# Kernel optimization log

Hardware: AMD Instinct MI355X
Metric: run time of the kernel (lower is better)

## Reference

```python
import jax, jax.numpy as jnp
import numpy as np

NG, NPG, EPG = 64, 256, 2048        # graphs, nodes/graph, edges/graph
N, E = NG * NPG, NG * EPG
FN, FE, FG = 256, 64, 128           # node/edge/global feature dims
MSG_DIMS = [FE + 2 * FN + FG, 512, 512, 256]   # message_arch '512-512-256'
UPD_DIMS = [256 + FN + FG, 512, 256]           # node_arch '512-256'
N_EMB_G, OUT_NODE, OUT_ACT = 256, 64, 8


def _mlp(x, params):
    # Linear -> ReLU stack (Dropout is identity in eval mode)
    for w, b in params:
        x = jax.nn.relu(x @ w + b)
    return x


def setup_inputs():
    key = jax.random.key(0)
    ks = jax.random.split(key, 24)
    nodes = jax.random.normal(ks[0], (N, FN), jnp.float32)
    edge_attr = jax.random.normal(ks[1], (E, FE), jnp.float32)
    global_attr = jax.random.normal(ks[2], (NG, FG), jnp.float32)
    # edges are grouped by graph (matches repeat_interleave(global, num_edges))
    rng = np.random.default_rng(0)
    gid_e = np.repeat(np.arange(NG), EPG)
    src = gid_e * NPG + rng.integers(0, NPG, E)
    tgt = gid_e * NPG + rng.integers(0, NPG, E)
    edge_indices = jnp.asarray(np.stack([src, tgt]), jnp.int32)
    num_nodes = jnp.full((NG,), NPG, jnp.int32)
    num_edges = jnp.full((NG,), EPG, jnp.int32)
    batch_indices = jnp.asarray(np.repeat(np.arange(NG), NPG), jnp.int32)

    def lin(k, fi, fo):
        kw, kb = jax.random.split(k)
        lim = 1.0 / np.sqrt(fi)
        return (jax.random.uniform(kw, (fi, fo), jnp.float32, -lim, lim),
                jax.random.uniform(kb, (fo,), jnp.float32, -lim, lim))

    inp = dict(nodes=nodes, edge_attr=edge_attr, global_attr=global_attr,
               edge_indices=edge_indices, num_nodes=num_nodes,
               num_edges=num_edges, batch_indices=batch_indices)
    for i in range(3):
        w, b = lin(ks[3 + i], MSG_DIMS[i], MSG_DIMS[i + 1])
        inp[f'msg_w{i}'], inp[f'msg_b{i}'] = w, b
    for i in range(2):
        w, b = lin(ks[6 + i], UPD_DIMS[i], UPD_DIMS[i + 1])
        inp[f'upd_w{i}'], inp[f'upd_b{i}'] = w, b
    inp['glob_w'], inp['glob_b'] = lin(ks[8], UPD_DIMS[-1] + FG, N_EMB_G)
    inp['emb_w'], inp['emb_b'] = lin(ks[9], UPD_DIMS[-1], OUT_NODE)
    inp['act_w'], inp['act_b'] = lin(ks[10], N_EMB_G, OUT_ACT)
    return inp


def reference(nodes, edge_attr, global_attr, edge_indices, num_nodes,
              num_edges, batch_indices, msg_w0, msg_b0, msg_w1, msg_b1,
              msg_w2, msg_b2, upd_w0, upd_b0, upd_w1, upd_b1,
              glob_w, glob_b, emb_w, emb_b, act_w, act_b):
    n, e = nodes.shape[0], edge_indices.shape[1]
    ng = global_attr.shape[0]
    src, tgt = edge_indices[0], edge_indices[1]
    glob_e = jnp.repeat(global_attr, num_edges, axis=0, total_repeat_length=e)
    concat = jnp.concatenate([nodes[src], edge_attr, nodes[tgt], glob_e], axis=1)
    # message_nn ends with ReLU; outer F.relu is a no-op on non-neg values
    message = _mlp(concat, [(msg_w0, msg_b0), (msg_w1, msg_b1), (msg_w2, msg_b2)])
    # scatter_max into per-node slots; messages >= 0 so zeros init matches fill=0
    aggr = jnp.zeros((n, message.shape[1]), message.dtype).at[tgt].max(message)
    glob_n = jnp.repeat(global_attr, num_nodes, axis=0, total_repeat_length=n)
    h = _mlp(jnp.concatenate([nodes, aggr, glob_n], axis=1),
             [(upd_w0, upd_b0), (upd_w1, upd_b1)])
    agg_nodes = jnp.zeros((ng, h.shape[1]), h.dtype).at[batch_indices].max(h)
    g = jax.nn.relu(jnp.concatenate([agg_nodes, global_attr], axis=1) @ glob_w + glob_b)
    node_pred = jax.nn.relu(h @ emb_w + emb_b)
    action = jax.nn.softmax(g @ act_w + act_b, axis=1)
    return node_pred, action
```

## Files before the change

kernel.cpp:

```cpp
#include <hip/hip_runtime.h>
#include <hip/hip_bf16.h>

typedef unsigned short u16;
using u16x4 = __attribute__((ext_vector_type(4))) unsigned short;
using u16x8 = __attribute__((ext_vector_type(8))) unsigned short;
using u32x4 = __attribute__((ext_vector_type(4))) unsigned int;
using f32x4 = __attribute__((ext_vector_type(4))) float;
using bf16x8 = __attribute__((ext_vector_type(8))) __bf16;

#define TNG 64
#define TNN 16384
#define TNE 131072
#define TFN 256
#define TFE 64
#define TFG 128

__device__ __forceinline__ u16 f2bf(float f) {
    unsigned u = __float_as_uint(f);
    unsigned r = (u + 0x7FFFu + ((u >> 16) & 1u)) >> 16;
    return (u16)r;
}
__device__ __forceinline__ float b2f(u16 h) {
    return __uint_as_float(((unsigned)h) << 16);
}

__device__ __forceinline__ void gload_lds16(const u16* g, u16* l) {
    __builtin_amdgcn_global_load_lds(
        (const __attribute__((address_space(1))) void*)g,
        (__attribute__((address_space(3))) void*)l, 16, 0, 0);
}

__device__ __forceinline__ int xcd_swz(int bid, int nwg) {
    return (nwg & 7) == 0 ? (bid & 7) * (nwg >> 3) + (bid >> 3) : bid;
}


__global__ void cast_kernel(const float* __restrict__ in, u16* __restrict__ out, int n4) {
    int i = blockIdx.x * 256 + threadIdx.x;
    if (i >= n4) return;
    f32x4 v = *(const f32x4*)(in + (size_t)i * 4);
    u16x4 o;
    o.x = f2bf(v.x); o.y = f2bf(v.y); o.z = f2bf(v.z); o.w = f2bf(v.w);
    *(u16x4*)(out + (size_t)i * 4) = o;
}


struct PrepTab {
    const float* W[8];
    int out_off[8];
    int Nin[8], Nact[8], r0[8], Ksub[8], idx0[8];
};

__global__ void prep_weights_kernel(PrepTab tab, u16* __restrict__ wsbase, int total) {
    int gid = blockIdx.x * 256 + threadIdx.x;
    if (gid >= total) return;
    int i = 7;
#pragma unroll
    for (int j = 7; j > 0; --j)
        if (gid < tab.idx0[j]) i = j - 1;
    int loc = gid - tab.idx0[i];
    int ks = tab.Ksub[i];
    int n = loc / ks;
    int k = loc - n * ks;
    float v = (n < tab.Nact[i]) ? tab.W[i][(size_t)(tab.r0[i] + k) * tab.Nin[i] + n] : 0.0f;
    wsbase[tab.out_off[i] + loc] = f2bf(v);
}


template <int K, int NXSH, bool RELU, bool OUT_BF16>
__global__ __launch_bounds__(256) void gemm_bt_kernel(
    const u16* __restrict__ A, const u16* __restrict__ Bt,
    const float* __restrict__ bias, void* __restrict__ Cv,
    int Nout, int ldc) {
    __shared__ u16 As[128 * 32];
    __shared__ u16 Bs[128 * 32];
    const int w = xcd_swz(blockIdx.x, gridDim.x);
    const int bxi = w & ((1 << NXSH) - 1);
    const int byi = w >> NXSH;
    const int tid = threadIdx.x;
    const int wave = tid >> 6, lane = tid & 63;
    const int wr = wave >> 1, wc = wave & 1;
    const size_t brow = (size_t)byi * 128;
    const size_t bcol = (size_t)bxi * 128;
    const int srow = tid >> 2;
    const int qsrc = (tid & 3) ^ ((srow >> 1) & 3);
    const u16* aSrc = A + (brow + srow) * (size_t)K + qsrc * 8;
    const u16* bSrc = Bt + (bcol + srow) * (size_t)K + qsrc * 8;
    u16* aDst = &As[tid * 8];
    u16* bDst = &Bs[tid * 8];
    const size_t stepRows = (size_t)64 * K;

    f32x4 acc[4][4] = {};

#pragma unroll
    for (int k0 = 0; k0 < K; k0 += 32) {
        gload_lds16(aSrc + k0, aDst);
        gload_lds16(aSrc + stepRows + k0, aDst + 2048);
        gload_lds16(bSrc + k0, bDst);
        gload_lds16(bSrc + stepRows + k0, bDst + 2048);
        __syncthreads();
        bf16x8 af[4], bfv[4];
#pragma unroll
        for (int m = 0; m < 4; ++m) {
            const int row = wr * 64 + m * 16 + (lane & 15);
            const int slot = (lane >> 4) ^ ((row >> 1) & 3);
            af[m] = *(const bf16x8*)&As[row * 32 + slot * 8];
        }
#pragma unroll
        for (int n = 0; n < 4; ++n) {
            const int row = wc * 64 + n * 16 + (lane & 15);
            const int slot = (lane >> 4) ^ ((row >> 1) & 3);
            bfv[n] = *(const bf16x8*)&Bs[row * 32 + slot * 8];
        }
#pragma unroll
        for (int m = 0; m < 4; ++m)
#pragma unroll
            for (int n = 0; n < 4; ++n)
                acc[m][n] = __builtin_amdgcn_mfma_f32_16x16x32_bf16(af[m], bfv[n], acc[m][n], 0, 0, 0);
        __syncthreads();
    }

    const int rowSub = wr * 64 + (lane >> 4) * 4;
#pragma unroll
    for (int n = 0; n < 4; ++n) {
        const int col = (int)bcol + wc * 64 + n * 16 + (lane & 15);
        if (col >= Nout) continue;
        const float bv = bias ? bias[col] : 0.0f;
#pragma unroll
        for (int m = 0; m < 4; ++m) {
#pragma unroll
            for (int i = 0; i < 4; ++i) {
                float v = acc[m][n][i] + bv;
                if (RELU) v = fmaxf(v, 0.0f);
                size_t off = (brow + rowSub + m * 16 + i) * (size_t)ldc + col;
                if (OUT_BF16) ((u16*)Cv)[off] = f2bf(v);
                else ((float*)Cv)[off] = v;
            }
        }
    }
}


__global__ __launch_bounds__(256) void gemm_u0_kernel(
    const u16* __restrict__ nodes_bf, const u16* __restrict__ aggr,
    const u16* __restrict__ glob_bf, const u16* __restrict__ U0T,
    const float* __restrict__ bias, u16* __restrict__ C) {
    __shared__ u16 As[128 * 32];
    __shared__ u16 Bs[128 * 32];
    const int w = xcd_swz(blockIdx.x, gridDim.x);
    const int bxi = w & 3;
    const int byi = w >> 2;
    const int tid = threadIdx.x;
    const int wave = tid >> 6, lane = tid & 63;
    const int wr = wave >> 1, wc = wave & 1;
    const size_t brow = (size_t)byi * 128;
    const size_t bcol = (size_t)bxi * 128;
    const int srow = tid >> 2;
    const int scol = ((tid & 3) ^ ((srow >> 1) & 3)) * 8;
    const int r0i = (int)brow + srow;
    const u16* bSrc = U0T + (bcol + srow) * (size_t)640 + scol;
    u16* aDst = &As[tid * 8];
    u16* bDst = &Bs[tid * 8];

    f32x4 acc[4][4] = {};

#pragma unroll
    for (int k0 = 0; k0 < 640; k0 += 32) {
        const u16* p0;
        const u16* p1;
        if (k0 < 256) {
            p0 = nodes_bf + (size_t)r0i * 256 + k0 + scol;
            p1 = nodes_bf + (size_t)(r0i + 64) * 256 + k0 + scol;
        } else if (k0 < 512) {
            p0 = aggr + (size_t)r0i * 256 + (k0 - 256) + scol;
            p1 = aggr + (size_t)(r0i + 64) * 256 + (k0 - 256) + scol;
        } else {
            p0 = glob_bf + (size_t)(r0i >> 8) * 128 + (k0 - 512) + scol;
            p1 = glob_bf + (size_t)((r0i + 64) >> 8) * 128 + (k0 - 512) + scol;
        }
        gload_lds16(p0, aDst);
        gload_lds16(p1, aDst + 2048);
        gload_lds16(bSrc + k0, bDst);
        gload_lds16(bSrc + (size_t)64 * 640 + k0, bDst + 2048);
        __syncthreads();
        bf16x8 af[4], bfv[4];
#pragma unroll
        for (int m = 0; m < 4; ++m) {
            const int row = wr * 64 + m * 16 + (lane & 15);
            const int slot = (lane >> 4) ^ ((row >> 1) & 3);
            af[m] = *(const bf16x8*)&As[row * 32 + slot * 8];
        }
#pragma unroll
        for (int n = 0; n < 4; ++n) {
            const int row = wc * 64 + n * 16 + (lane & 15);
            const int slot = (lane >> 4) ^ ((row >> 1) & 3);
            bfv[n] = *(const bf16x8*)&Bs[row * 32 + slot * 8];
        }
#pragma unroll
        for (int m = 0; m < 4; ++m)
#pragma unroll
            for (int n = 0; n < 4; ++n)
                acc[m][n] = __builtin_amdgcn_mfma_f32_16x16x32_bf16(af[m], bfv[n], acc[m][n], 0, 0, 0);
        __syncthreads();
    }

    const int rowSub = wr * 64 + (lane >> 4) * 4;
#pragma unroll
    for (int n = 0; n < 4; ++n) {
        const int col = (int)bcol + wc * 64 + n * 16 + (lane & 15);
        const float bv = bias[col];
#pragma unroll
        for (int m = 0; m < 4; ++m)
#pragma unroll
            for (int i = 0; i < 4; ++i) {
                float v = fmaxf(acc[m][n][i] + bv, 0.0f);
                C[(brow + rowSub + m * 16 + i) * (size_t)512 + col] = f2bf(v);
            }
    }
}


__global__ __launch_bounds__(256) void gd_kernel(const float* __restrict__ glob,
                                                 const float* __restrict__ msg_w0,
                                                 const float* __restrict__ b0,
                                                 float* __restrict__ Gdb,
                                                 u16* __restrict__ glob_bf) {
    int g = blockIdx.x;
    __shared__ float in[TFG];
    if (threadIdx.x < TFG) {
        float v = glob[g * TFG + threadIdx.x];
        in[threadIdx.x] = v;
        glob_bf[g * TFG + threadIdx.x] = f2bf(v);
    }
    __syncthreads();
    for (int j = threadIdx.x; j < 512; j += 256) {
        float s = b0[j];
        for (int k = 0; k < TFG; ++k) s += in[k] * msg_w0[(size_t)(576 + k) * 512 + j];
        Gdb[(size_t)g * 512 + j] = s;
    }
}


__global__ __launch_bounds__(256) void h1_fused_kernel(
    const float* __restrict__ Ef, const u16* __restrict__ WbT,
    const u16* __restrict__ Pac, const float* __restrict__ Gdb,
    const int* __restrict__ src, const int* __restrict__ tgt,
    u16* __restrict__ h1, int e0) {
    __shared__ u16 smem[17408];
    u16* As = smem;
    u16* Bs = smem + 8192;
    const int w = xcd_swz(blockIdx.x, gridDim.x);
    const int bxi = w & 3;
    const int byi = w >> 2;
    const int tid = threadIdx.x;
    const int wave = tid >> 6, lane = tid & 63;
    const int wr = wave >> 1, wc = wave & 1;
    const int brow = byi * 128;
    const int bcol = bxi * 128;

    {
        const int r = tid >> 2;
        const int cq = (tid & 3) * 2;
        const int sw = r & 7;
#pragma unroll
        for (int h = 0; h < 2; ++h) {
            const float* sp = Ef + (size_t)(e0 + brow + r + h * 64) * 64 + cq * 8;
            f32x4 v0 = *(const f32x4*)(sp);
            f32x4 v1 = *(const f32x4*)(sp + 4);
            f32x4 v2 = *(const f32x4*)(sp + 8);
            f32x4 v3 = *(const f32x4*)(sp + 12);
            u16x8 o0, o1;
            o0[0] = f2bf(v0.x); o0[1] = f2bf(v0.y); o0[2] = f2bf(v0.z); o0[3] = f2bf(v0.w);
            o0[4] = f2bf(v1.x); o0[5] = f2bf(v1.y); o0[6] = f2bf(v1.z); o0[7] = f2bf(v1.w);
            o1[0] = f2bf(v2.x); o1[1] = f2bf(v2.y); o1[2] = f2bf(v2.z); o1[3] = f2bf(v2.w);
            o1[4] = f2bf(v3.x); o1[5] = f2bf(v3.y); o1[6] = f2bf(v3.z); o1[7] = f2bf(v3.w);
            *(u16x8*)&As[(r + h * 64) * 64 + (cq ^ sw) * 8] = o0;
            *(u16x8*)&As[(r + h * 64) * 64 + ((cq + 1) ^ sw) * 8] = o1;
        }
#pragma unroll
        for (int j = 0; j < 4; ++j) {
            int li = j * 256 + tid;
            int row = li >> 3;
            int gslot = (li & 7) ^ (row & 7);
            gload_lds16(WbT + (size_t)(bcol + row) * 64 + gslot * 8, &Bs[li * 8]);
        }
    }
    __syncthreads();

    f32x4 acc[4][4] = {};
#pragma unroll
    for (int k0 = 0; k0 < 64; k0 += 32) {
        bf16x8 af[4], bv[4];
#pragma unroll
        for (int m = 0; m < 4; ++m) {
            const int row = wr * 64 + m * 16 + (lane & 15);
            const int slot = ((k0 >> 3) + (lane >> 4)) ^ (row & 7);
            af[m] = *(const bf16x8*)&As[row * 64 + slot * 8];
        }
#pragma unroll
        for (int n = 0; n < 4; ++n) {
            const int row = wc * 64 + n * 16 + (lane & 15);
            const int slot = ((k0 >> 3) + (lane >> 4)) ^ (row & 7);
            bv[n] = *(const bf16x8*)&Bs[row * 64 + slot * 8];
        }
#pragma unroll
        for (int m = 0; m < 4; ++m)
#pragma unroll
            for (int n = 0; n < 4; ++n)
                acc[m][n] = __builtin_amdgcn_mfma_f32_16x16x32_bf16(af[m], bv[n], acc[m][n], 0, 0, 0);
    }
    __syncthreads();

    const int rowSub = wr * 64 + (lane >> 4) * 4;
#pragma unroll
    for (int m = 0; m < 4; ++m)
#pragma unroll
        for (int n = 0; n < 4; ++n)
#pragma unroll
            for (int i = 0; i < 4; ++i)
                smem[(rowSub + m * 16 + i) * 136 + wc * 64 + n * 16 + (lane & 15)] =
                    f2bf(acc[m][n][i]);
    __syncthreads();

#pragma unroll
    for (int it = 0; it < 8; ++it) {
        int lin = it * 256 + tid;
        int r = lin >> 4;
        int q = (lin & 15) * 8;
        int e = e0 + brow + r;
        int s = src[e];
        int t = tgt[e];
        int g = e >> 11;
        int col = bcol + q;
        u16x8 pa = *(const u16x8*)(Pac + (size_t)s * 1024 + col);
        u16x8 pc = *(const u16x8*)(Pac + (size_t)t * 1024 + 512 + col);
        u16x8 eb = *(const u16x8*)&smem[r * 136 + q];
        f32x4 g0 = *(const f32x4*)(Gdb + (size_t)g * 512 + col);
        f32x4 g1 = *(const f32x4*)(Gdb + (size_t)g * 512 + col + 4);
        u16x8 o;
#pragma unroll
        for (int j = 0; j < 8; ++j) {
            float gd = (j < 4) ? g0[j] : g1[j - 4];
            float v = b2f(pa[j]) + b2f(pc[j]) + b2f(eb[j]) + gd;
            o[j] = f2bf(fmaxf(v, 0.0f));
        }
        *(u16x8*)(h1 + (size_t)(brow + r) * 512 + col) = o;
    }
}


__global__ __launch_bounds__(1024) void scatter_max_kernel(
    const u16* __restrict__ msg, const int* __restrict__ tgt,
    u16* __restrict__ aggr, int g0, int e0) {
    int g = g0 + (blockIdx.x >> 2);
    int fc = blockIdx.x & 3;
    __shared__ unsigned smax[256 * 64];
    int tid = threadIdx.x;
    for (int i = tid; i < 256 * 64; i += 1024) smax[i] = 0u;
    __syncthreads();
    const int eg = g * 2048;
    const int n0 = g * 256;
    const int f = tid & 63;
    const int eo = tid >> 6;
    const u16* mrow = msg + fc * 64 + f;
    const int end = eg + 2048;
    for (int e = eg + eo; e < end; e += 64) {
        int t0 = tgt[e], t1 = tgt[e + 16], t2 = tgt[e + 32], t3 = tgt[e + 48];
        unsigned v0 = ((unsigned)mrow[(size_t)(e      - e0) * 256]) << 16;
        unsigned v1 = ((unsigned)mrow[(size_t)(e + 16 - e0) * 256]) << 16;
        unsigned v2 = ((unsigned)mrow[(size_t)(e + 32 - e0) * 256]) << 16;
        unsigned v3 = ((unsigned)mrow[(size_t)(e + 48 - e0) * 256]) << 16;
        int a0 = t0 - n0, a1 = t1 - n0, a2 = t2 - n0, a3 = t3 - n0;
        if ((unsigned)a0 < 256u) atomicMax(&smax[a0 * 64 + f], v0);
        if ((unsigned)a1 < 256u) atomicMax(&smax[a1 * 64 + f], v1);
        if ((unsigned)a2 < 256u) atomicMax(&smax[a2 * 64 + f], v2);
        if ((unsigned)a3 < 256u) atomicMax(&smax[a3 * 64 + f], v3);
    }
    __syncthreads();
    for (int i = tid; i < 256 * 64; i += 1024) {
        int nl = i >> 6, ff = i & 63;
        aggr[(size_t)(n0 + nl) * 256 + fc * 64 + ff] = (u16)(smax[nl * 64 + ff] >> 16);
    }
}


__global__ __launch_bounds__(256) void agg_nodes_kernel(
    const u16* __restrict__ h, float* __restrict__ aggn) {
    int g = blockIdx.x;
    int f = threadIdx.x;
    int n0 = g * 256;
    float m0 = 0.0f, m1 = 0.0f, m2 = 0.0f, m3 = 0.0f;
    for (int n = 0; n < 256; n += 4) {
        m0 = fmaxf(m0, b2f(h[(size_t)(n0 + n) * 256 + f]));
        m1 = fmaxf(m1, b2f(h[(size_t)(n0 + n + 1) * 256 + f]));
        m2 = fmaxf(m2, b2f(h[(size_t)(n0 + n + 2) * 256 + f]));
        m3 = fmaxf(m3, b2f(h[(size_t)(n0 + n + 3) * 256 + f]));
    }
    aggn[(size_t)g * 256 + f] = fmaxf(fmaxf(m0, m1), fmaxf(m2, m3));
}


__global__ __launch_bounds__(256) void glob_kernel(
    const float* __restrict__ aggn, const float* __restrict__ glob,
    const float* __restrict__ W, const float* __restrict__ b,
    float* __restrict__ gout) {
    int g = blockIdx.x;
    int j = threadIdx.x;
    __shared__ float in[384];
    if (threadIdx.x < 256) in[threadIdx.x] = aggn[(size_t)g * 256 + threadIdx.x];
    if (threadIdx.x < 128) in[256 + threadIdx.x] = glob[(size_t)g * 128 + threadIdx.x];
    __syncthreads();
    float s = b[j];
    for (int k = 0; k < 384; ++k) s += in[k] * W[(size_t)k * 256 + j];
    gout[(size_t)g * 256 + j] = fmaxf(s, 0.0f);
}


__global__ void action_kernel(const float* __restrict__ gout,
                              const float* __restrict__ actw,
                              const float* __restrict__ actb,
                              float* __restrict__ out) {
    int g = blockIdx.x;
    int j = threadIdx.x;
    __shared__ float logits[8];
    if (j < 8) {
        float s = actb[j];
        for (int k = 0; k < 256; ++k) s += gout[(size_t)g * 256 + k] * actw[(size_t)k * 8 + j];
        logits[j] = s;
    }
    __syncthreads();
    if (j == 0) {
        float mx = logits[0];
        for (int i = 1; i < 8; ++i) mx = fmaxf(mx, logits[i]);
        float ex[8], den = 0.0f;
        for (int i = 0; i < 8; ++i) { ex[i] = expf(logits[i] - mx); den += ex[i]; }
        float inv = 1.0f / den;
        for (int i = 0; i < 8; ++i) out[(size_t)g * 8 + i] = ex[i] * inv;
    }
}


constexpr size_t OFF_NODES_BF = 0;
constexpr size_t OFF_GLOB_BF  = OFF_NODES_BF + (size_t)TNN * TFN * 2;
constexpr size_t OFF_WACT = OFF_GLOB_BF + (size_t)TNG * TFG * 2;
constexpr size_t OFF_WBT  = OFF_WACT + 1024 * 256 * 2;
constexpr size_t OFF_W1T  = OFF_WBT + 512 * 64 * 2;
constexpr size_t OFF_W2T  = OFF_W1T + 512 * 512 * 2;
constexpr size_t OFF_U0T  = OFF_W2T + 256 * 512 * 2;
constexpr size_t OFF_U1T  = OFF_U0T + 512 * 640 * 2;
constexpr size_t OFF_EMBT = OFF_U1T + 256 * 512 * 2;
constexpr size_t OFF_AGGN = OFF_EMBT + 128 * 256 * 2;
constexpr size_t OFF_GOUT = OFF_AGGN + 64 * 256 * 4;
constexpr size_t OFF_AGGR = OFF_GOUT + 64 * 256 * 4;
constexpr size_t OFF_GDB  = OFF_AGGR + (size_t)TNN * 256 * 2;
constexpr size_t OFF_PAC  = OFF_GDB + 64 * 512 * 4;
constexpr size_t OFF_V    = OFF_PAC + (size_t)TNN * 1024 * 2;
constexpr size_t SZ_HU1   = (size_t)TNN * 512 * 2;

extern "C" void kernel_launch(void* const* d_in, const int* in_sizes, int n_in,
                              void* d_out, int out_size, void* d_ws, size_t ws_size,
                              hipStream_t stream) {
    const float* nodes       = (const float*)d_in[0];
    const float* edge_attr   = (const float*)d_in[1];
    const float* global_attr = (const float*)d_in[2];
    const int*   edge_idx    = (const int*)d_in[3];
    const float* msg_w0 = (const float*)d_in[7];
    const float* msg_b0 = (const float*)d_in[8];
    const float* msg_w1 = (const float*)d_in[9];
    const float* msg_b1 = (const float*)d_in[10];
    const float* msg_w2 = (const float*)d_in[11];
    const float* msg_b2 = (const float*)d_in[12];
    const float* upd_w0 = (const float*)d_in[13];
    const float* upd_b0 = (const float*)d_in[14];
    const float* upd_w1 = (const float*)d_in[15];
    const float* upd_b1 = (const float*)d_in[16];
    const float* glob_w = (const float*)d_in[17];
    const float* glob_b = (const float*)d_in[18];
    const float* emb_w  = (const float*)d_in[19];
    const float* emb_b  = (const float*)d_in[20];
    const float* act_w  = (const float*)d_in[21];
    const float* act_b  = (const float*)d_in[22];

    const int* src = edge_idx;
    const int* tgt = edge_idx + TNE;

    char* ws = (char*)d_ws;
    u16* nodes_bf = (u16*)(ws + OFF_NODES_BF);
    u16* glob_bf  = (u16*)(ws + OFF_GLOB_BF);
    u16* WacT = (u16*)(ws + OFF_WACT);
    u16* WbT  = (u16*)(ws + OFF_WBT);
    u16* W1T  = (u16*)(ws + OFF_W1T);
    u16* W2T  = (u16*)(ws + OFF_W2T);
    u16* U0T  = (u16*)(ws + OFF_U0T);
    u16* U1T  = (u16*)(ws + OFF_U1T);
    u16* EmbT = (u16*)(ws + OFF_EMBT);
    float* aggn = (float*)(ws + OFF_AGGN);
    float* gout = (float*)(ws + OFF_GOUT);
    u16* aggr = (u16*)(ws + OFF_AGGR);
    float* Gdb = (float*)(ws + OFF_GDB);
    u16* Pac  = (u16*)(ws + OFF_PAC);
    float* out = (float*)d_out;

    size_t CH = (size_t)TNE;
    while (CH > 2048) {
        size_t need = OFF_V + (CH * 2560 > SZ_HU1 ? CH * 2560 : SZ_HU1);
        if (need <= ws_size) break;
        CH >>= 1;
    }
    const int nchunk = (int)((size_t)TNE / CH);
    const int gpc = (int)(CH / 2048);

    u16* h1c  = (u16*)(ws + OFF_V);
    u16* h2c  = (u16*)(ws + OFF_V + CH * 1024);
    u16* msgc = (u16*)(ws + OFF_V + CH * 2048);
    u16* hu1  = (u16*)(ws + OFF_V);
    u16* h_bf = (u16*)(ws + OFF_AGGR);

    cast_kernel<<<(TNN * TFN / 4 + 255) / 256, 256, 0, stream>>>(nodes, nodes_bf, TNN * TFN / 4);

    PrepTab tab;
    {
        const float* Ws[8]  = {msg_w0, msg_w0, msg_w0, msg_w1, msg_w2, upd_w0, upd_w1, emb_w};
        int offs[8] = {(int)(OFF_WACT / 2), (int)(OFF_WACT / 2) + 131072, (int)(OFF_WBT / 2),
                       (int)(OFF_W1T / 2), (int)(OFF_W2T / 2), (int)(OFF_U0T / 2),
                       (int)(OFF_U1T / 2), (int)(OFF_EMBT / 2)};
        int nin[8]  = {512, 512, 512, 512, 256, 512, 256, 64};
        int nact[8] = {512, 512, 512, 512, 256, 512, 256, 64};
        int r0v[8]  = {0, 320, 256, 0, 0, 0, 0, 0};
        int ksub[8] = {256, 256, 64, 512, 512, 640, 512, 256};
        int sizes[8] = {131072, 131072, 32768, 262144, 131072, 327680, 131072, 32768};
        int acc = 0;
        for (int i = 0; i < 8; ++i) {
            tab.W[i] = Ws[i]; tab.out_off[i] = offs[i]; tab.Nin[i] = nin[i];
            tab.Nact[i] = nact[i]; tab.r0[i] = r0v[i]; tab.Ksub[i] = ksub[i];
            tab.idx0[i] = acc; acc += sizes[i];
        }
    }
    prep_weights_kernel<<<4608, 256, 0, stream>>>(tab, (u16*)ws, 1179648);
    gd_kernel<<<64, 256, 0, stream>>>(global_attr, msg_w0, msg_b0, Gdb, glob_bf);

    gemm_bt_kernel<256, 3, false, true><<<1024, 256, 0, stream>>>(nodes_bf, WacT, nullptr, Pac, 1024, 1024);

    for (int ci = 0; ci < nchunk; ++ci) {
        const int e0 = (int)(ci * CH);
        const int nwg = (int)(CH / 32);
        h1_fused_kernel<<<nwg, 256, 0, stream>>>(
            edge_attr, WbT, Pac, Gdb, src, tgt, h1c, e0);
        gemm_bt_kernel<512, 2, true, true><<<nwg, 256, 0, stream>>>(h1c, W1T, msg_b1, h2c, 512, 512);
        gemm_bt_kernel<512, 1, true, true><<<nwg / 2, 256, 0, stream>>>(h2c, W2T, msg_b2, msgc, 256, 256);
        scatter_max_kernel<<<gpc * 4, 1024, 0, stream>>>(msgc, tgt, aggr, ci * gpc, e0);
    }

    gemm_u0_kernel<<<512, 256, 0, stream>>>(nodes_bf, aggr, glob_bf, U0T, upd_b0, hu1);
    gemm_bt_kernel<512, 1, true, true><<<256, 256, 0, stream>>>(hu1, U1T, upd_b1, h_bf, 256, 256);

    agg_nodes_kernel<<<64, 256, 0, stream>>>(h_bf, aggn);
    glob_kernel<<<64, 256, 0, stream>>>(aggn, global_attr, glob_w, glob_b, gout);
    action_kernel<<<64, 64, 0, stream>>>(gout, act_w, act_b, out + (size_t)TNN * 64);
    gemm_bt_kernel<256, 0, true, false><<<128, 256, 0, stream>>>(h_bf, EmbT, emb_b, out, 64, 64);

    (void)in_sizes; (void)n_in; (void)out_size;
}
```

Measured before the change: 400.3 us.

## Double-buffer GEMM LDS tiles, tile weight prep, vectorize scatter, fuse head kernels

The bf16 GEMM kernels, including the fused update GEMM, now use two LDS buffers. The next K-slice is loaded while MFMAs run on the current one, which is meant to hide global-load latency behind compute. Weight preparation becomes a 64x64 LDS-tiled transpose so both reads and writes are coalesced, instead of one strided gather per element. scatter_max reads four message features per thread with a vector load. The three small head kernels (node max-pool, global MLP, softmax) are merged into one, which removes two launches and their intermediate buffers. The cost is twice the LDS per GEMM block, which may lower occupancy.

```diff
diff --git a/kernel.cpp b/kernel.cpp
--- a/kernel.cpp
+++ b/kernel.cpp
@@ -48,22 +48,39 @@
 struct PrepTab {
     const float* W[8];
     int out_off[8];
-    int Nin[8], Nact[8], r0[8], Ksub[8], idx0[8];
+    int Nin[8], Nact[8], r0[8], Ksub[8];
+    int tile0[8];
+    int tkn[8];
 };
 
-__global__ void prep_weights_kernel(PrepTab tab, u16* __restrict__ wsbase, int total) {
-    int gid = blockIdx.x * 256 + threadIdx.x;
-    if (gid >= total) return;
+__global__ __launch_bounds__(256) void prep_weights_kernel(PrepTab tab, u16* __restrict__ wsbase) {
+    const int b = blockIdx.x;
     int i = 7;
 #pragma unroll
     for (int j = 7; j > 0; --j)
-        if (gid < tab.idx0[j]) i = j - 1;
-    int loc = gid - tab.idx0[i];
-    int ks = tab.Ksub[i];
-    int n = loc / ks;
-    int k = loc - n * ks;
-    float v = (n < tab.Nact[i]) ? tab.W[i][(size_t)(tab.r0[i] + k) * tab.Nin[i] + n] : 0.0f;
-    wsbase[tab.out_off[i] + loc] = f2bf(v);
+        if (b < tab.tile0[j]) i = j - 1;
+    const int loc = b - tab.tile0[i];
+    const int tk = loc % tab.tkn[i];
+    const int tn = loc / tab.tkn[i];
+    const int kb = tk * 64, nb = tn * 64;
+    const int Nin = tab.Nin[i], Nact = tab.Nact[i], r0 = tab.r0[i], Ksub = tab.Ksub[i];
+    const float* W = tab.W[i];
+    u16* outp = wsbase + tab.out_off[i];
+
+    __shared__ float t[64][65];
+    const int tid = threadIdx.x;
+    const int nl = tid & 63;
+    const bool nok = (nb + nl) < Nact;
+#pragma unroll 4
+    for (int kk = tid >> 6; kk < 64; kk += 4) {
+        float v = nok ? W[(size_t)(r0 + kb + kk) * Nin + nb + nl] : 0.0f;
+        t[kk][nl] = v;
+    }
+    __syncthreads();
+    const int kl = tid & 63;
+#pragma unroll 4
+    for (int nn = tid >> 6; nn < 64; nn += 4)
+        outp[(size_t)(nb + nn) * Ksub + kb + kl] = f2bf(t[kl][nn]);
 }
 
 
@@ -72,8 +89,9 @@
     const u16* __restrict__ A, const u16* __restrict__ Bt,
     const float* __restrict__ bias, void* __restrict__ Cv,
     int Nout, int ldc) {
-    __shared__ u16 As[128 * 32];
-    __shared__ u16 Bs[128 * 32];
+    constexpr int NT = K / 32;
+    __shared__ u16 As[2][4096];
+    __shared__ u16 Bs[2][4096];
     const int w = xcd_swz(blockIdx.x, gridDim.x);
     const int bxi = w & ((1 << NXSH) - 1);
     const int byi = w >> NXSH;
@@ -86,31 +104,36 @@
     const int qsrc = (tid & 3) ^ ((srow >> 1) & 3);
     const u16* aSrc = A + (brow + srow) * (size_t)K + qsrc * 8;
     const u16* bSrc = Bt + (bcol + srow) * (size_t)K + qsrc * 8;
-    u16* aDst = &As[tid * 8];
-    u16* bDst = &Bs[tid * 8];
     const size_t stepRows = (size_t)64 * K;
 
+    auto stage = [&](int t, int buf) {
+        const int k0 = t * 32;
+        gload_lds16(aSrc + k0, &As[buf][tid * 8]);
+        gload_lds16(aSrc + stepRows + k0, &As[buf][tid * 8 + 2048]);
+        gload_lds16(bSrc + k0, &Bs[buf][tid * 8]);
+        gload_lds16(bSrc + stepRows + k0, &Bs[buf][tid * 8 + 2048]);
+    };
+
     f32x4 acc[4][4] = {};
 
-#pragma unroll
-    for (int k0 = 0; k0 < K; k0 += 32) {
-        gload_lds16(aSrc + k0, aDst);
-        gload_lds16(aSrc + stepRows + k0, aDst + 2048);
-        gload_lds16(bSrc + k0, bDst);
-        gload_lds16(bSrc + stepRows + k0, bDst + 2048);
-        __syncthreads();
+    stage(0, 0);
+    __syncthreads();
+#pragma unroll
+    for (int t = 0; t < NT; ++t) {
+        const int cur = t & 1;
+        if (t + 1 < NT) stage(t + 1, cur ^ 1);
         bf16x8 af[4], bfv[4];
 #pragma unroll
         for (int m = 0; m < 4; ++m) {
             const int row = wr * 64 + m * 16 + (lane & 15);
             const int slot = (lane >> 4) ^ ((row >> 1) & 3);
-            af[m] = *(const bf16x8*)&As[row * 32 + slot * 8];
+            af[m] = *(const bf16x8*)&As[cur][row * 32 + slot * 8];
         }
 #pragma unroll
         for (int n = 0; n < 4; ++n) {
             const int row = wc * 64 + n * 16 + (lane & 15);
             const int slot = (lane >> 4) ^ ((row >> 1) & 3);
-            bfv[n] = *(const bf16x8*)&Bs[row * 32 + slot * 8];
+            bfv[n] = *(const bf16x8*)&Bs[cur][row * 32 + slot * 8];
         }
 #pragma unroll
         for (int m = 0; m < 4; ++m)
@@ -145,8 +168,8 @@
     const u16* __restrict__ nodes_bf, const u16* __restrict__ aggr,
     const u16* __restrict__ glob_bf, const u16* __restrict__ U0T,
     const float* __restrict__ bias, u16* __restrict__ C) {
-    __shared__ u16 As[128 * 32];
-    __shared__ u16 Bs[128 * 32];
+    __shared__ u16 As[2][4096];
+    __shared__ u16 Bs[2][4096];
     const int w = xcd_swz(blockIdx.x, gridDim.x);
     const int bxi = w & 3;
     const int byi = w >> 2;
@@ -159,15 +182,10 @@
     const int scol = ((tid & 3) ^ ((srow >> 1) & 3)) * 8;
     const int r0i = (int)brow + srow;
     const u16* bSrc = U0T + (bcol + srow) * (size_t)640 + scol;
-    u16* aDst = &As[tid * 8];
-    u16* bDst = &Bs[tid * 8];
-
-    f32x4 acc[4][4] = {};
-
-#pragma unroll
-    for (int k0 = 0; k0 < 640; k0 += 32) {
-        const u16* p0;
-        const u16* p1;
+
+    auto stage = [&](int t, int buf) {
+        const int k0 = t * 32;
+        const u16 *p0, *p1;
         if (k0 < 256) {
             p0 = nodes_bf + (size_t)r0i * 256 + k0 + scol;
             p1 = nodes_bf + (size_t)(r0i + 64) * 256 + k0 + scol;
@@ -178,23 +196,32 @@
             p0 = glob_bf + (size_t)(r0i >> 8) * 128 + (k0 - 512) + scol;
             p1 = glob_bf + (size_t)((r0i + 64) >> 8) * 128 + (k0 - 512) + scol;
         }
-        gload_lds16(p0, aDst);
-        gload_lds16(p1, aDst + 2048);
-        gload_lds16(bSrc + k0, bDst);
-        gload_lds16(bSrc + (size_t)64 * 640 + k0, bDst + 2048);
-        __syncthreads();
+        gload_lds16(p0, &As[buf][tid * 8]);
+        gload_lds16(p1, &As[buf][tid * 8 + 2048]);
+        gload_lds16(bSrc + k0, &Bs[buf][tid * 8]);
+        gload_lds16(bSrc + (size_t)64 * 640 + k0, &Bs[buf][tid * 8 + 2048]);
+    };
+
+    f32x4 acc[4][4] = {};
+
+    stage(0, 0);
+    __syncthreads();
+#pragma unroll
+    for (int t = 0; t < 20; ++t) {
+        const int cur = t & 1;
+        if (t + 1 < 20) stage(t + 1, cur ^ 1);
         bf16x8 af[4], bfv[4];
 #pragma unroll
         for (int m = 0; m < 4; ++m) {
             const int row = wr * 64 + m * 16 + (lane & 15);
             const int slot = (lane >> 4) ^ ((row >> 1) & 3);
-            af[m] = *(const bf16x8*)&As[row * 32 + slot * 8];
+            af[m] = *(const bf16x8*)&As[cur][row * 32 + slot * 8];
         }
 #pragma unroll
         for (int n = 0; n < 4; ++n) {
             const int row = wc * 64 + n * 16 + (lane & 15);
             const int slot = (lane >> 4) ^ ((row >> 1) & 3);
-            bfv[n] = *(const bf16x8*)&Bs[row * 32 + slot * 8];
+            bfv[n] = *(const bf16x8*)&Bs[cur][row * 32 + slot * 8];
         }
 #pragma unroll
         for (int m = 0; m < 4; ++m)
@@ -360,21 +387,42 @@
     __syncthreads();
     const int eg = g * 2048;
     const int n0 = g * 256;
-    const int f = tid & 63;
-    const int eo = tid >> 6;
-    const u16* mrow = msg + fc * 64 + f;
-    const int end = eg + 2048;
-    for (int e = eg + eo; e < end; e += 64) {
-        int t0 = tgt[e], t1 = tgt[e + 16], t2 = tgt[e + 32], t3 = tgt[e + 48];
-        unsigned v0 = ((unsigned)mrow[(size_t)(e      - e0) * 256]) << 16;
-        unsigned v1 = ((unsigned)mrow[(size_t)(e + 16 - e0) * 256]) << 16;
-        unsigned v2 = ((unsigned)mrow[(size_t)(e + 32 - e0) * 256]) << 16;
-        unsigned v3 = ((unsigned)mrow[(size_t)(e + 48 - e0) * 256]) << 16;
+    const int f4 = (tid & 15) * 4;
+    const int elane = tid >> 4;
+    const u16* mbase = msg + fc * 64 + f4;
+#pragma unroll
+    for (int wv = 0; wv < 32; wv += 4) {
+        const int e = eg + elane + wv * 64;
+        int t0 = tgt[e], t1 = tgt[e + 64], t2 = tgt[e + 128], t3 = tgt[e + 192];
+        u16x4 m0 = *(const u16x4*)(mbase + (size_t)(e       - e0) * 256);
+        u16x4 m1 = *(const u16x4*)(mbase + (size_t)(e +  64 - e0) * 256);
+        u16x4 m2 = *(const u16x4*)(mbase + (size_t)(e + 128 - e0) * 256);
+        u16x4 m3 = *(const u16x4*)(mbase + (size_t)(e + 192 - e0) * 256);
         int a0 = t0 - n0, a1 = t1 - n0, a2 = t2 - n0, a3 = t3 - n0;
-        if ((unsigned)a0 < 256u) atomicMax(&smax[a0 * 64 + f], v0);
-        if ((unsigned)a1 < 256u) atomicMax(&smax[a1 * 64 + f], v1);
-        if ((unsigned)a2 < 256u) atomicMax(&smax[a2 * 64 + f], v2);
-        if ((unsigned)a3 < 256u) atomicMax(&smax[a3 * 64 + f], v3);
+        if ((unsigned)a0 < 256u) {
+            atomicMax(&smax[a0 * 64 + f4],     ((unsigned)m0.x) << 16);
+            atomicMax(&smax[a0 * 64 + f4 + 1], ((unsigned)m0.y) << 16);
+            atomicMax(&smax[a0 * 64 + f4 + 2], ((unsigned)m0.z) << 16);
+            atomicMax(&smax[a0 * 64 + f4 + 3], ((unsigned)m0.w) << 16);
+        }
+        if ((unsigned)a1 < 256u) {
+            atomicMax(&smax[a1 * 64 + f4],     ((unsigned)m1.x) << 16);
+            atomicMax(&smax[a1 * 64 + f4 + 1], ((unsigned)m1.y) << 16);
+            atomicMax(&smax[a1 * 64 + f4 + 2], ((unsigned)m1.z) << 16);
+            atomicMax(&smax[a1 * 64 + f4 + 3], ((unsigned)m1.w) << 16);
+        }
+        if ((unsigned)a2 < 256u) {
+            atomicMax(&smax[a2 * 64 + f4],     ((unsigned)m2.x) << 16);
+            atomicMax(&smax[a2 * 64 + f4 + 1], ((unsigned)m2.y) << 16);
+            atomicMax(&smax[a2 * 64 + f4 + 2], ((unsigned)m2.z) << 16);
+            atomicMax(&smax[a2 * 64 + f4 + 3], ((unsigned)m2.w) << 16);
+        }
+        if ((unsigned)a3 < 256u) {
+            atomicMax(&smax[a3 * 64 + f4],     ((unsigned)m3.x) << 16);
+            atomicMax(&smax[a3 * 64 + f4 + 1], ((unsigned)m3.y) << 16);
+            atomicMax(&smax[a3 * 64 + f4 + 2], ((unsigned)m3.z) << 16);
+            atomicMax(&smax[a3 * 64 + f4 + 3], ((unsigned)m3.w) << 16);
+        }
     }
     __syncthreads();
     for (int i = tid; i < 256 * 64; i += 1024) {
@@ -384,58 +432,48 @@
 }
 
 
-__global__ __launch_bounds__(256) void agg_nodes_kernel(
-    const u16* __restrict__ h, float* __restrict__ aggn) {
+__global__ __launch_bounds__(256) void head_kernel(
+    const u16* __restrict__ h, const float* __restrict__ glob,
+    const float* __restrict__ W, const float* __restrict__ b,
+    const float* __restrict__ actw, const float* __restrict__ actb,
+    float* __restrict__ out_act) {
     int g = blockIdx.x;
-    int f = threadIdx.x;
-    int n0 = g * 256;
-    float m0 = 0.0f, m1 = 0.0f, m2 = 0.0f, m3 = 0.0f;
-    for (int n = 0; n < 256; n += 4) {
-        m0 = fmaxf(m0, b2f(h[(size_t)(n0 + n) * 256 + f]));
-        m1 = fmaxf(m1, b2f(h[(size_t)(n0 + n + 1) * 256 + f]));
-        m2 = fmaxf(m2, b2f(h[(size_t)(n0 + n + 2) * 256 + f]));
-        m3 = fmaxf(m3, b2f(h[(size_t)(n0 + n + 3) * 256 + f]));
-    }
-    aggn[(size_t)g * 256 + f] = fmaxf(fmaxf(m0, m1), fmaxf(m2, m3));
-}
-
-
-__global__ __launch_bounds__(256) void glob_kernel(
-    const float* __restrict__ aggn, const float* __restrict__ glob,
-    const float* __restrict__ W, const float* __restrict__ b,
-    float* __restrict__ gout) {
-    int g = blockIdx.x;
-    int j = threadIdx.x;
+    int tid = threadIdx.x;
     __shared__ float in[384];
-    if (threadIdx.x < 256) in[threadIdx.x] = aggn[(size_t)g * 256 + threadIdx.x];
-    if (threadIdx.x < 128) in[256 + threadIdx.x] = glob[(size_t)g * 128 + threadIdx.x];
-    __syncthreads();
-    float s = b[j];
-    for (int k = 0; k < 384; ++k) s += in[k] * W[(size_t)k * 256 + j];
-    gout[(size_t)g * 256 + j] = fmaxf(s, 0.0f);
-}
-
-
-__global__ void action_kernel(const float* __restrict__ gout,
-                              const float* __restrict__ actw,
-                              const float* __restrict__ actb,
-                              float* __restrict__ out) {
-    int g = blockIdx.x;
-    int j = threadIdx.x;
+    __shared__ float go[256];
     __shared__ float logits[8];
-    if (j < 8) {
-        float s = actb[j];
-        for (int k = 0; k < 256; ++k) s += gout[(size_t)g * 256 + k] * actw[(size_t)k * 8 + j];
-        logits[j] = s;
-    }
-    __syncthreads();
-    if (j == 0) {
+    {
+        const size_t base = (size_t)g * 256 * 256 + tid;
+        float m0 = 0.0f, m1 = 0.0f, m2 = 0.0f, m3 = 0.0f;
+        for (int n = 0; n < 256; n += 4) {
+            m0 = fmaxf(m0, b2f(h[base + (size_t)n * 256]));
+            m1 = fmaxf(m1, b2f(h[base + (size_t)(n + 1) * 256]));
+            m2 = fmaxf(m2, b2f(h[base + (size_t)(n + 2) * 256]));
+            m3 = fmaxf(m3, b2f(h[base + (size_t)(n + 3) * 256]));
+        }
+        in[tid] = fmaxf(fmaxf(m0, m1), fmaxf(m2, m3));
+        if (tid < 128) in[256 + tid] = glob[(size_t)g * 128 + tid];
+    }
+    __syncthreads();
+    {
+        float s = b[tid];
+        for (int k = 0; k < 384; ++k) s += in[k] * W[(size_t)k * 256 + tid];
+        go[tid] = fmaxf(s, 0.0f);
+    }
+    __syncthreads();
+    if (tid < 8) {
+        float s = actb[tid];
+        for (int k = 0; k < 256; ++k) s += go[k] * actw[(size_t)k * 8 + tid];
+        logits[tid] = s;
+    }
+    __syncthreads();
+    if (tid == 0) {
         float mx = logits[0];
         for (int i = 1; i < 8; ++i) mx = fmaxf(mx, logits[i]);
         float ex[8], den = 0.0f;
         for (int i = 0; i < 8; ++i) { ex[i] = expf(logits[i] - mx); den += ex[i]; }
         float inv = 1.0f / den;
-        for (int i = 0; i < 8; ++i) out[(size_t)g * 8 + i] = ex[i] * inv;
+        for (int i = 0; i < 8; ++i) out_act[(size_t)g * 8 + i] = ex[i] * inv;
     }
 }
 
@@ -449,9 +487,7 @@
 constexpr size_t OFF_U0T  = OFF_W2T + 256 * 512 * 2;
 constexpr size_t OFF_U1T  = OFF_U0T + 512 * 640 * 2;
 constexpr size_t OFF_EMBT = OFF_U1T + 256 * 512 * 2;
-constexpr size_t OFF_AGGN = OFF_EMBT + 128 * 256 * 2;
-constexpr size_t OFF_GOUT = OFF_AGGN + 64 * 256 * 4;
-constexpr size_t OFF_AGGR = OFF_GOUT + 64 * 256 * 4;
+constexpr size_t OFF_AGGR = OFF_EMBT + 128 * 256 * 2;
 constexpr size_t OFF_GDB  = OFF_AGGR + (size_t)TNN * 256 * 2;
 constexpr size_t OFF_PAC  = OFF_GDB + 64 * 512 * 4;
 constexpr size_t OFF_V    = OFF_PAC + (size_t)TNN * 1024 * 2;
@@ -494,8 +530,6 @@
     u16* U0T  = (u16*)(ws + OFF_U0T);
     u16* U1T  = (u16*)(ws + OFF_U1T);
     u16* EmbT = (u16*)(ws + OFF_EMBT);
-    float* aggn = (float*)(ws + OFF_AGGN);
-    float* gout = (float*)(ws + OFF_GOUT);
     u16* aggr = (u16*)(ws + OFF_AGGR);
     float* Gdb = (float*)(ws + OFF_GDB);
     u16* Pac  = (u16*)(ws + OFF_PAC);
@@ -519,6 +553,7 @@
     cast_kernel<<<(TNN * TFN / 4 + 255) / 256, 256, 0, stream>>>(nodes, nodes_bf, TNN * TFN / 4);
 
     PrepTab tab;
+    int ntiles = 0;
     {
         const float* Ws[8]  = {msg_w0, msg_w0, msg_w0, msg_w1, msg_w2, upd_w0, upd_w1, emb_w};
         int offs[8] = {(int)(OFF_WACT / 2), (int)(OFF_WACT / 2) + 131072, (int)(OFF_WBT / 2),
@@ -528,15 +563,18 @@
         int nact[8] = {512, 512, 512, 512, 256, 512, 256, 64};
         int r0v[8]  = {0, 320, 256, 0, 0, 0, 0, 0};
         int ksub[8] = {256, 256, 64, 512, 512, 640, 512, 256};
-        int sizes[8] = {131072, 131072, 32768, 262144, 131072, 327680, 131072, 32768};
+        int npad[8] = {512, 512, 512, 512, 256, 512, 256, 128};
         int acc = 0;
         for (int i = 0; i < 8; ++i) {
             tab.W[i] = Ws[i]; tab.out_off[i] = offs[i]; tab.Nin[i] = nin[i];
             tab.Nact[i] = nact[i]; tab.r0[i] = r0v[i]; tab.Ksub[i] = ksub[i];
-            tab.idx0[i] = acc; acc += sizes[i];
-        }
-    }
-    prep_weights_kernel<<<4608, 256, 0, stream>>>(tab, (u16*)ws, 1179648);
+            tab.tkn[i] = ksub[i] / 64;
+            tab.tile0[i] = acc;
+            acc += (npad[i] / 64) * (ksub[i] / 64);
+        }
+        ntiles = acc;
+    }
+    prep_weights_kernel<<<ntiles, 256, 0, stream>>>(tab, (u16*)ws);
     gd_kernel<<<64, 256, 0, stream>>>(global_attr, msg_w0, msg_b0, Gdb, glob_bf);
 
     gemm_bt_kernel<256, 3, false, true><<<1024, 256, 0, stream>>>(nodes_bf, WacT, nullptr, Pac, 1024, 1024);
@@ -554,9 +592,8 @@
     gemm_u0_kernel<<<512, 256, 0, stream>>>(nodes_bf, aggr, glob_bf, U0T, upd_b0, hu1);
     gemm_bt_kernel<512, 1, true, true><<<256, 256, 0, stream>>>(hu1, U1T, upd_b1, h_bf, 256, 256);
 
-    agg_nodes_kernel<<<64, 256, 0, stream>>>(h_bf, aggn);
-    glob_kernel<<<64, 256, 0, stream>>>(aggn, global_attr, glob_w, glob_b, gout);
-    action_kernel<<<64, 64, 0, stream>>>(gout, act_w, act_b, out + (size_t)TNN * 64);
+    head_kernel<<<64, 256, 0, stream>>>(h_bf, global_attr, glob_w, glob_b,
+                                        act_w, act_b, out + (size_t)TNN * 64);
     gemm_bt_kernel<256, 0, true, false><<<128, 256, 0, stream>>>(h_bf, EmbT, emb_b, out, 64, 64);
 
     (void)in_sizes; (void)n_in; (void)out_size;
```

Measured after the change: 371.7 us. 1.08x faster.
